# Kernel optimization log

Measured on AMD Instinct MI355X. Metric: run time of the kernel, lower is better.

## Reference

```python
import jax, jax.numpy as jnp
import numpy as np

N = 32768   # nodes
D = 16      # fixed in-degree (neighbors per node)
C = 128     # in_channels
H = 128     # hidden_channels (out of each SAGEConv)


def setup_inputs() -> dict:
    key = jax.random.key(0)
    ks = jax.random.split(key, 20)
    x = jax.random.normal(ks[0], (N, C), dtype=jnp.float32)
    # edges sorted by destination, exactly D neighbors per node (PyG
    # LSTMAggregation requires dst-sorted edge_index)
    src = jax.random.randint(ks[1], (N * D,), 0, N, dtype=jnp.int32)
    dst = jnp.repeat(jnp.arange(N, dtype=jnp.int32), D)
    edge_index = jnp.stack([src, dst])  # [2, E]

    s = 1.0 / np.sqrt(C)
    def mat(k, o, i):
        return jax.random.uniform(k, (o, i), jnp.float32, -s, s)
    def vec(k, o):
        return jax.random.uniform(k, (o,), jnp.float32, -s, s)

    inp = {"x": x, "edge_index": edge_index}
    for k0, base in [(2, "conv1"), (10, "conv2")]:
        inp[f"{base}_wih"] = mat(ks[k0 + 0], 4 * C, C)   # LSTM input weights
        inp[f"{base}_whh"] = mat(ks[k0 + 1], 4 * C, C)   # LSTM hidden weights
        inp[f"{base}_bih"] = vec(ks[k0 + 2], 4 * C)
        inp[f"{base}_bhh"] = vec(ks[k0 + 3], 4 * C)
        inp[f"{base}_wl"] = mat(ks[k0 + 4], H, C)        # lin_l (neighbor branch, has bias)
        inp[f"{base}_bl"] = vec(ks[k0 + 5], H)
        inp[f"{base}_wr"] = mat(ks[k0 + 6], H, C)        # lin_r (root branch, no bias)
    return inp


def _lstm_last(seq, wih, whh, bih, bhh):
    # seq: [D, N, C]. PyTorch LSTM, gate order (i, f, g, o).
    # PyG LSTMAggregation returns lstm(x)[0][:, -1] == hidden state at the
    # last (padded) timestep; here every node has exactly D real neighbors.
    n = seq.shape[1]
    h0 = jnp.zeros((n, wih.shape[0] // 4), seq.dtype)
    b = bih + bhh

    def step(carry, x_t):
        h, c = carry
        g = x_t @ wih.T + h @ whh.T + b            # [N, 4H]
        i, f, gg, o = jnp.split(g, 4, axis=-1)
        c = jax.nn.sigmoid(f) * c + jax.nn.sigmoid(i) * jnp.tanh(gg)
        h = jax.nn.sigmoid(o) * jnp.tanh(c)
        return (h, c), None

    (h, _), _ = jax.lax.scan(step, (h0, h0), seq)
    return h


def _sage_conv(x, src, wih, whh, bih, bhh, wl, bl, wr):
    n, c = x.shape
    d = src.shape[0] // n
    # dense neighbor batch [N, D, C]: edges are dst-sorted with fixed degree,
    # so the gather reshapes directly (== PyG to_dense_batch)
    msgs = x[src].reshape(n, d, c)
    aggr = _lstm_last(jnp.swapaxes(msgs, 0, 1), wih, whh, bih, bhh)  # [N, C]
    return aggr @ wl.T + bl + x @ wr.T


def reference(x, edge_index,
              conv1_wih, conv1_whh, conv1_bih, conv1_bhh, conv1_wl, conv1_bl, conv1_wr,
              conv2_wih, conv2_whh, conv2_bih, conv2_bhh, conv2_wl, conv2_bl, conv2_wr):
    src = edge_index[0]
    h = _sage_conv(x, src, conv1_wih, conv1_whh, conv1_bih, conv1_bhh,
                   conv1_wl, conv1_bl, conv1_wr)
    h = jax.nn.relu(h)
    out = _sage_conv(h, src, conv2_wih, conv2_whh, conv2_bih, conv2_bhh,
                     conv2_wl, conv2_bl, conv2_wr)
    return out
```

## Files before the change

kernel.cpp:

```cpp
#include <hip/hip_runtime.h>
#include <stdint.h>

#define NN 32768
#define DEG 16
#define CH 128
#define G4 512
#define MB 64

typedef short bf16x8 __attribute__((ext_vector_type(8)));
typedef float f32x4 __attribute__((ext_vector_type(4)));
typedef unsigned short u16;
typedef u16 u16x8 __attribute__((ext_vector_type(8)));
typedef uint32_t u32;

#define L2E 1.4426950408889634f

__device__ __forceinline__ u16 f2bf(float f) {
  union { float f; uint32_t u; } v; v.f = f;
  uint32_t u = v.u;
  return (u16)((u + 0x7FFFu + ((u >> 16) & 1u)) >> 16);
}

__device__ __forceinline__ float exp2f_fast(float x) {
#if __has_builtin(__builtin_amdgcn_exp2f)
  return __builtin_amdgcn_exp2f(x);
#else
  float r; asm("v_exp_f32 %0, %1" : "=v"(r) : "v"(x)); return r;
#endif
}
__device__ __forceinline__ float rcpf_fast(float x) {
#if __has_builtin(__builtin_amdgcn_rcpf)
  return __builtin_amdgcn_rcpf(x);
#else
  float r; asm("v_rcp_f32 %0, %1" : "=v"(r) : "v"(x)); return r;
#endif
}
__device__ __forceinline__ u32 cvtpk(float lo, float hi) {
  u32 r; asm("v_cvt_pk_bf16_f32 %0, %1, %2" : "=v"(r) : "v"(lo), "v"(hi));
  return r;
}

__global__ void k_cvt_bf16(const float* __restrict__ in, u16* __restrict__ out, int n8) {
  int i = blockIdx.x * blockDim.x + threadIdx.x;
  if (i >= n8) return;
  const float* pp = in + (size_t)i * 8;
  u16x8 o;
  #pragma unroll
  for (int j = 0; j < 8; ++j) o[j] = f2bf(pp[j]);
  *(u16x8*)(out + (size_t)i * 8) = o;
}

__global__ void k_pack_lstm(const float* __restrict__ wih, const float* __restrict__ whh,
                            const float* __restrict__ bih, const float* __restrict__ bhh,
                            u16* __restrict__ Wc, float* __restrict__ bs) {
  int idx = blockIdx.x * blockDim.x + threadIdx.x;
  int g = idx >> 8, k = idx & 255;
  int gate = g >> 7;
  float sc = (gate == 2) ? (2.0f * L2E) : L2E;
  float v = (k < CH) ? wih[g * CH + k] : whh[g * CH + (k - CH)];
  Wc[g * 256 + k] = f2bf(v * sc);
  if (k == 0) {
    float b = (bih[g] + bhh[g]) * sc;
    bs[g] = (gate == 2) ? b : -b;
  }
}

__global__ void k_pack_lin(const float* __restrict__ wl, const float* __restrict__ wr,
                           u16* __restrict__ W) {
  int idx = blockIdx.x * blockDim.x + threadIdx.x;
  int o = idx >> 8, k = idx & 255;
  float v = (k < CH) ? wl[o * CH + k] : wr[o * CH + (k - CH)];
  W[o * 256 + k] = f2bf(v);
}

__global__ __launch_bounds__(512, 2)
void k_lstm(const u16* __restrict__ xin, const int* __restrict__ src,
            const u16* __restrict__ Wc, const float* __restrict__ bs,
            u16* __restrict__ aggr) {
  __shared__ u16 xh[MB * 256];
  __shared__ int srcs[MB * DEG];
  const int tid = threadIdx.x;
  const int lane = tid & 63;
  const int wave = tid >> 6;
  const int l15 = lane & 15;
  const int lg  = lane >> 4;
  const int nodeBase = blockIdx.x * MB;

  srcs[tid]       = src[nodeBase * DEG + tid];
  srcs[tid + 512] = src[nodeBase * DEG + tid + 512];

  bf16x8 Wf[4][8];
  {
    const u16* wp = Wc + (wave * 16 + l15) * 256 + lg * 8;
    #pragma unroll
    for (int gt = 0; gt < 4; ++gt)
      #pragma unroll
      for (int kt = 0; kt < 8; ++kt)
        Wf[gt][kt] = *(const bf16x8*)(wp + gt * (CH * 256) + kt * 32);
  }
  const float bi = bs[0 * CH + wave * 16 + l15];
  const float bf = bs[1 * CH + wave * 16 + l15];
  const float bg = bs[2 * CH + wave * 16 + l15];
  const float bo = bs[3 * CH + wave * 16 + l15];

  const int s_swz = (l15 & 7) << 4;
  int abase[4];
  #pragma unroll
  for (int mt = 0; mt < 4; ++mt)
    abase[mt] = (mt * 16 + l15) * 512 + ((lg * 16) ^ s_swz);
  int haddr[4];
  #pragma unroll
  for (int q = 0; q < 4; ++q)
    haddr[q] = (lg * 4 + q) * 512 +
               ((256 + wave * 32 + l15 * 2) ^ ((((lg & 1) * 4) + q) << 4));
  const int r  = tid >> 4;
  const int ck = (tid & 15) << 4;
  const int stg  = r * 512 + (ck ^ ((r & 7) << 4));
  const int stgH = r * 512 + ((256 + ck) ^ ((r & 7) << 4));
  const int sidx = r * DEG;

  __syncthreads();
  {
    int s0 = srcs[sidx];
    int s1 = srcs[sidx + 32 * DEG];
    bf16x8 v0 = *(const bf16x8*)(xin + (size_t)s0 * CH + (ck >> 1));
    bf16x8 v1 = *(const bf16x8*)(xin + (size_t)s1 * CH + (ck >> 1));
    *(bf16x8*)((char*)xh + stg)          = v0;
    *(bf16x8*)((char*)xh + stg + 16384)  = v1;
    bf16x8 z = {};
    *(bf16x8*)((char*)xh + stgH)         = z;
    *(bf16x8*)((char*)xh + stgH + 16384) = z;
  }

  float cst[4][4] = {{0.f}};
  u32 hp[4][2];
  const f32x4 zero4 = {0.f, 0.f, 0.f, 0.f};

  #pragma unroll 1
  for (int t = 0; t < DEG; ++t) {
    __syncthreads();
    bf16x8 xp0 = {}, xp1 = {};
    if (t + 1 < DEG) {
      int s0 = srcs[sidx + t + 1];
      int s1 = srcs[sidx + 32 * DEG + t + 1];
      xp0 = *(const bf16x8*)(xin + (size_t)s0 * CH + (ck >> 1));
      xp1 = *(const bf16x8*)(xin + (size_t)s1 * CH + (ck >> 1));
    }
    f32x4 acc[2][4];
    #pragma unroll
    for (int mt = 0; mt < 4; ++mt) {
      const int pp = mt & 1;
      #pragma unroll
      for (int kt = 0; kt < 8; ++kt) {
        bf16x8 A = *(const bf16x8*)((char*)xh + (abase[mt] ^ (kt * 64)));
        if (kt == 0) {
          #pragma unroll
          for (int gt = 0; gt < 4; ++gt)
            acc[pp][gt] = __builtin_amdgcn_mfma_f32_16x16x32_bf16(A, Wf[gt][0], zero4, 0, 0, 0);
        } else {
          #pragma unroll
          for (int gt = 0; gt < 4; ++gt)
            acc[pp][gt] = __builtin_amdgcn_mfma_f32_16x16x32_bf16(A, Wf[gt][kt], acc[pp][gt], 0, 0, 0);
        }
      }
      float hq[4];
      #pragma unroll
      for (int q = 0; q < 4; ++q) {
        float si = rcpf_fast(1.0f + exp2f_fast(bi - acc[pp][0][q]));
        float sf = rcpf_fast(1.0f + exp2f_fast(bf - acc[pp][1][q]));
        float so = rcpf_fast(1.0f + exp2f_fast(bo - acc[pp][3][q]));
        float gg = fmaf(-2.0f, rcpf_fast(1.0f + exp2f_fast(acc[pp][2][q] + bg)), 1.0f);
        float c  = fmaf(sf, cst[mt][q], si * gg);
        cst[mt][q] = c;
        float tc = fmaf(-2.0f, rcpf_fast(1.0f + exp2f_fast(c * 2.8853900817779268f)), 1.0f);
        hq[q] = so * tc;
      }
      hp[mt][0] = cvtpk(hq[0], hq[1]);
      hp[mt][1] = cvtpk(hq[2], hq[3]);
    }
    __syncthreads();
    if (t + 1 < DEG) {
      #pragma unroll
      for (int mt = 0; mt < 4; ++mt) {
        *(u16*)((char*)xh + haddr[0] + mt * 8192) = (u16)(hp[mt][0]);
        *(u16*)((char*)xh + haddr[1] + mt * 8192) = (u16)(hp[mt][0] >> 16);
        *(u16*)((char*)xh + haddr[2] + mt * 8192) = (u16)(hp[mt][1]);
        *(u16*)((char*)xh + haddr[3] + mt * 8192) = (u16)(hp[mt][1] >> 16);
      }
      *(bf16x8*)((char*)xh + stg)         = xp0;
      *(bf16x8*)((char*)xh + stg + 16384) = xp1;
    }
  }

  #pragma unroll
  for (int mt = 0; mt < 4; ++mt) {
    size_t rowb = (size_t)(nodeBase + mt * 16 + lg * 4);
    u16* op = aggr + rowb * CH + wave * 16 + l15;
    op[0 * CH] = (u16)(hp[mt][0]);
    op[1 * CH] = (u16)(hp[mt][0] >> 16);
    op[2 * CH] = (u16)(hp[mt][1]);
    op[3 * CH] = (u16)(hp[mt][1] >> 16);
  }
}

__global__ __launch_bounds__(256, 4)
void k_linear(const u16* __restrict__ aggr, const u16* __restrict__ xroot,
              const u16* __restrict__ W, const float* __restrict__ bl,
              u16* __restrict__ out_bf, float* __restrict__ out_f, int relu) {
  const int lane = threadIdx.x & 63;
  const int wave = threadIdx.x >> 6;
  const int l15 = lane & 15, lg = lane >> 4;
  const int rowBase = blockIdx.x * 64 + wave * 16;

  f32x4 acc[8];
  #pragma unroll
  for (int nt = 0; nt < 8; ++nt) {
    float b = bl[nt * 16 + l15];
    acc[nt] = { b, b, b, b };
  }
  #pragma unroll
  for (int kt = 0; kt < 8; ++kt) {
    const u16* ap = (kt < 4) ? (aggr  + (size_t)(rowBase + l15) * CH + kt * 32 + lg * 8)
                             : (xroot + (size_t)(rowBase + l15) * CH + (kt - 4) * 32 + lg * 8);
    bf16x8 A = *(const bf16x8*)ap;
    #pragma unroll
    for (int nt = 0; nt < 8; ++nt) {
      bf16x8 B = *(const bf16x8*)(W + (nt * 16 + l15) * 256 + kt * 32 + lg * 8);
      acc[nt] = __builtin_amdgcn_mfma_f32_16x16x32_bf16(A, B, acc[nt], 0, 0, 0);
    }
  }
  #pragma unroll
  for (int nt = 0; nt < 8; ++nt) {
    #pragma unroll
    for (int q = 0; q < 4; ++q) {
      float v = acc[nt][q];
      if (relu) v = fmaxf(v, 0.0f);
      int row = rowBase + lg * 4 + q;
      int col = nt * 16 + l15;
      if (out_bf) out_bf[(size_t)row * CH + col] = f2bf(v);
      else        out_f[(size_t)row * CH + col]  = v;
    }
  }
}

extern "C" void kernel_launch(void* const* d_in, const int* in_sizes, int n_in,
                              void* d_out, int out_size, void* d_ws, size_t ws_size,
                              hipStream_t stream) {
  (void)in_sizes; (void)n_in; (void)out_size; (void)ws_size;
  const float* x    = (const float*)d_in[0];
  const int*   ei   = (const int*)d_in[1];
  const float* w1ih = (const float*)d_in[2];
  const float* w1hh = (const float*)d_in[3];
  const float* b1ih = (const float*)d_in[4];
  const float* b1hh = (const float*)d_in[5];
  const float* w1l  = (const float*)d_in[6];
  const float* b1l  = (const float*)d_in[7];
  const float* w1r  = (const float*)d_in[8];
  const float* w2ih = (const float*)d_in[9];
  const float* w2hh = (const float*)d_in[10];
  const float* b2ih = (const float*)d_in[11];
  const float* b2hh = (const float*)d_in[12];
  const float* w2l  = (const float*)d_in[13];
  const float* b2l  = (const float*)d_in[14];
  const float* w2r  = (const float*)d_in[15];

  char* p = (char*)d_ws;
  u16* x_bf  = (u16*)p;  p += (size_t)NN * CH * 2;
  u16* h1_bf = (u16*)p;  p += (size_t)NN * CH * 2;
  u16* ag_bf = (u16*)p;  p += (size_t)NN * CH * 2;
  u16* Wc1   = (u16*)p;  p += G4 * 256 * 2;
  u16* Wc2   = (u16*)p;  p += G4 * 256 * 2;
  u16* Wl1   = (u16*)p;  p += CH * 256 * 2;
  u16* Wl2   = (u16*)p;  p += CH * 256 * 2;
  float* bs1 = (float*)p; p += G4 * 4;
  float* bs2 = (float*)p; p += G4 * 4;

  k_cvt_bf16<<<(NN * CH / 8 + 255) / 256, 256, 0, stream>>>(x, x_bf, NN * CH / 8);
  k_pack_lstm<<<G4, 256, 0, stream>>>(w1ih, w1hh, b1ih, b1hh, Wc1, bs1);
  k_pack_lstm<<<G4, 256, 0, stream>>>(w2ih, w2hh, b2ih, b2hh, Wc2, bs2);
  k_pack_lin<<<CH, 256, 0, stream>>>(w1l, w1r, Wl1);
  k_pack_lin<<<CH, 256, 0, stream>>>(w2l, w2r, Wl2);

  k_lstm<<<NN / MB, 512, 0, stream>>>(x_bf, ei, Wc1, bs1, ag_bf);
  k_linear<<<NN / 64, 256, 0, stream>>>(ag_bf, x_bf, Wl1, b1l, h1_bf, nullptr, 1);
  k_lstm<<<NN / MB, 512, 0, stream>>>(h1_bf, ei, Wc2, bs2, ag_bf);
  k_linear<<<NN / 64, 256, 0, stream>>>(ag_bf, h1_bf, Wl2, b2l, nullptr, (float*)d_out, 0);
}
```

Baseline: 319.1 us.

## Double-buffer LSTM LDS tile to drop one barrier per timestep

Doubles the shared-memory x/h staging buffer so each timestep reads one buffer while writing the next step's hidden state and gathered neighbor features into the other. This removes the second __syncthreads per step and lets each gate block's h be stored as soon as it is computed. The gate bias is folded into the first MFMA accumulator, and s_setprio raises priority around the MFMA loops. The cost is double the LDS per block, which may limit occupancy, plus a fully unrolled macro body that adds code size.

```diff
diff --git a/kernel.cpp b/kernel.cpp
--- a/kernel.cpp
+++ b/kernel.cpp
@@ -6,6 +6,7 @@
 #define CH 128
 #define G4 512
 #define MB 64
+#define BUF 32768
 
 typedef short bf16x8 __attribute__((ext_vector_type(8)));
 typedef float f32x4 __attribute__((ext_vector_type(4)));
@@ -13,14 +14,14 @@
 typedef u16 u16x8 __attribute__((ext_vector_type(8)));
 typedef uint32_t u32;
 
-#define L2E 1.4426950408889634f
+#define L2E  1.4426950408889634f
+#define L2E2 2.8853900817779268f
 
 __device__ __forceinline__ u16 f2bf(float f) {
   union { float f; uint32_t u; } v; v.f = f;
   uint32_t u = v.u;
   return (u16)((u + 0x7FFFu + ((u >> 16) & 1u)) >> 16);
 }
-
 __device__ __forceinline__ float exp2f_fast(float x) {
 #if __has_builtin(__builtin_amdgcn_exp2f)
   return __builtin_amdgcn_exp2f(x);
@@ -56,13 +57,10 @@
   int idx = blockIdx.x * blockDim.x + threadIdx.x;
   int g = idx >> 8, k = idx & 255;
   int gate = g >> 7;
-  float sc = (gate == 2) ? (2.0f * L2E) : L2E;
+  float sc = (gate == 2) ? L2E2 : L2E;
   float v = (k < CH) ? wih[g * CH + k] : whh[g * CH + (k - CH)];
   Wc[g * 256 + k] = f2bf(v * sc);
-  if (k == 0) {
-    float b = (bih[g] + bhh[g]) * sc;
-    bs[g] = (gate == 2) ? b : -b;
-  }
+  if (k == 0) bs[g] = (bih[g] + bhh[g]) * sc;
 }
 
 __global__ void k_pack_lin(const float* __restrict__ wl, const float* __restrict__ wr,
@@ -73,12 +71,76 @@
   W[o * 256 + k] = f2bf(v);
 }
 
+#define LSTM_BODY(T, RD, WR, ISLAST) do {                                      \
+  __syncthreads();                                                             \
+  bf16x8 xp0 = {}, xp1 = {};                                                   \
+  if (!(ISLAST)) {                                                             \
+    int s0_ = srcs[sidx + (T) + 1];                                            \
+    int s1_ = srcs[sidx + 32 * DEG + (T) + 1];                                 \
+    xp0 = *(const bf16x8*)(xin + (size_t)s0_ * CH + ckh);                      \
+    xp1 = *(const bf16x8*)(xin + (size_t)s1_ * CH + ckh);                      \
+  }                                                                            \
+  _Pragma("unroll")                                                            \
+  for (int mt = 0; mt < 4; ++mt) {                                             \
+    const int pp = mt & 1;                                                     \
+    __builtin_amdgcn_s_setprio(1);                                             \
+    _Pragma("unroll")                                                          \
+    for (int kt = 0; kt < 8; ++kt) {                                           \
+      const bf16x8 A = *(const bf16x8*)(xhb + ((kt & 1) ? aB : aA)             \
+                        + ((RD) + mt * 8192 + (kt >> 1) * 128));               \
+      if (kt == 0) {                                                           \
+        _Pragma("unroll")                                                      \
+        for (int gt = 0; gt < 4; ++gt)                                         \
+          acc[pp][gt] = __builtin_amdgcn_mfma_f32_16x16x32_bf16(               \
+              A, Wf[gt][0], bias[gt], 0, 0, 0);                                \
+      } else {                                                                 \
+        _Pragma("unroll")                                                      \
+        for (int gt = 0; gt < 4; ++gt)                                         \
+          acc[pp][gt] = __builtin_amdgcn_mfma_f32_16x16x32_bf16(               \
+              A, Wf[gt][kt], acc[pp][gt], 0, 0, 0);                            \
+      }                                                                        \
+    }                                                                          \
+    __builtin_amdgcn_s_setprio(0);                                             \
+    float hq[4];                                                               \
+    _Pragma("unroll")                                                          \
+    for (int q = 0; q < 4; ++q) {                                              \
+      float si = rcpf_fast(1.0f + exp2f_fast(-acc[pp][0][q]));                 \
+      float sf = rcpf_fast(1.0f + exp2f_fast(-acc[pp][1][q]));                 \
+      float so = rcpf_fast(1.0f + exp2f_fast(-acc[pp][3][q]));                 \
+      float gg = fmaf(-2.0f, rcpf_fast(1.0f + exp2f_fast(acc[pp][2][q])), 1.0f); \
+      float c  = fmaf(sf, cst[mt][q], si * gg);                                \
+      cst[mt][q] = c;                                                          \
+      float tc = fmaf(-2.0f, rcpf_fast(1.0f + exp2f_fast(c * L2E2)), 1.0f);    \
+      hq[q] = so * tc;                                                         \
+    }                                                                          \
+    u32 hp0 = cvtpk(hq[0], hq[1]);                                             \
+    u32 hp1 = cvtpk(hq[2], hq[3]);                                             \
+    if (!(ISLAST)) {                                                           \
+      *(u16*)(xhb + h0a + ((WR) + mt * 8192)) = (u16)hp0;                      \
+      *(u16*)(xhb + h1a + ((WR) + mt * 8192)) = (u16)(hp0 >> 16);              \
+      *(u16*)(xhb + h2a + ((WR) + mt * 8192)) = (u16)hp1;                      \
+      *(u16*)(xhb + h3a + ((WR) + mt * 8192)) = (u16)(hp1 >> 16);              \
+    } else {                                                                   \
+      u16* op_ = aggrp + mt * 16 * CH;                                         \
+      op_[0 * CH] = (u16)hp0;                                                  \
+      op_[1 * CH] = (u16)(hp0 >> 16);                                          \
+      op_[2 * CH] = (u16)hp1;                                                  \
+      op_[3 * CH] = (u16)(hp1 >> 16);                                          \
+    }                                                                          \
+  }                                                                            \
+  if (!(ISLAST)) {                                                             \
+    *(bf16x8*)(xhb + stg + (WR))         = xp0;                                \
+    *(bf16x8*)(xhb + stg + (WR) + 16384) = xp1;                                \
+  }                                                                            \
+} while (0)
+
 __global__ __launch_bounds__(512, 2)
 void k_lstm(const u16* __restrict__ xin, const int* __restrict__ src,
             const u16* __restrict__ Wc, const float* __restrict__ bs,
             u16* __restrict__ aggr) {
-  __shared__ u16 xh[MB * 256];
+  __shared__ u16 xh[2 * MB * 256];
   __shared__ int srcs[MB * DEG];
+  char* xhb = (char*)xh;
   const int tid = threadIdx.x;
   const int lane = tid & 63;
   const int wave = tid >> 6;
@@ -98,109 +160,51 @@
       for (int kt = 0; kt < 8; ++kt)
         Wf[gt][kt] = *(const bf16x8*)(wp + gt * (CH * 256) + kt * 32);
   }
-  const float bi = bs[0 * CH + wave * 16 + l15];
-  const float bf = bs[1 * CH + wave * 16 + l15];
-  const float bg = bs[2 * CH + wave * 16 + l15];
-  const float bo = bs[3 * CH + wave * 16 + l15];
-
-  const int s_swz = (l15 & 7) << 4;
-  int abase[4];
-  #pragma unroll
-  for (int mt = 0; mt < 4; ++mt)
-    abase[mt] = (mt * 16 + l15) * 512 + ((lg * 16) ^ s_swz);
-  int haddr[4];
-  #pragma unroll
-  for (int q = 0; q < 4; ++q)
-    haddr[q] = (lg * 4 + q) * 512 +
-               ((256 + wave * 32 + l15 * 2) ^ ((((lg & 1) * 4) + q) << 4));
-  const int r  = tid >> 4;
-  const int ck = (tid & 15) << 4;
+  f32x4 bias[4];
+  #pragma unroll
+  for (int gt = 0; gt < 4; ++gt) {
+    float b = bs[gt * CH + wave * 16 + l15];
+    bias[gt] = { b, b, b, b };
+  }
+
+  const int aA = l15 * 512 + ((lg * 16) ^ ((l15 & 7) << 4));
+  const int aB = aA ^ 64;
+  const int hcol = 256 + wave * 32 + l15 * 2;
+  const int h0a = (lg * 4 + 0) * 512 + (hcol ^ ((((lg & 1) * 4) + 0) << 4));
+  const int h1a = (lg * 4 + 1) * 512 + (hcol ^ ((((lg & 1) * 4) + 1) << 4));
+  const int h2a = (lg * 4 + 2) * 512 + (hcol ^ ((((lg & 1) * 4) + 2) << 4));
+  const int h3a = (lg * 4 + 3) * 512 + (hcol ^ ((((lg & 1) * 4) + 3) << 4));
+  const int r   = tid >> 4;
+  const int ck  = (tid & 15) << 4;
+  const int ckh = (tid & 15) * 8;
   const int stg  = r * 512 + (ck ^ ((r & 7) << 4));
   const int stgH = r * 512 + ((256 + ck) ^ ((r & 7) << 4));
   const int sidx = r * DEG;
+  u16* aggrp = aggr + (size_t)(nodeBase + lg * 4) * CH + wave * 16 + l15;
 
   __syncthreads();
   {
     int s0 = srcs[sidx];
     int s1 = srcs[sidx + 32 * DEG];
-    bf16x8 v0 = *(const bf16x8*)(xin + (size_t)s0 * CH + (ck >> 1));
-    bf16x8 v1 = *(const bf16x8*)(xin + (size_t)s1 * CH + (ck >> 1));
-    *(bf16x8*)((char*)xh + stg)          = v0;
-    *(bf16x8*)((char*)xh + stg + 16384)  = v1;
+    bf16x8 v0 = *(const bf16x8*)(xin + (size_t)s0 * CH + ckh);
+    bf16x8 v1 = *(const bf16x8*)(xin + (size_t)s1 * CH + ckh);
+    *(bf16x8*)(xhb + stg)          = v0;
+    *(bf16x8*)(xhb + stg + 16384)  = v1;
     bf16x8 z = {};
-    *(bf16x8*)((char*)xh + stgH)         = z;
-    *(bf16x8*)((char*)xh + stgH + 16384) = z;
+    *(bf16x8*)(xhb + stgH)         = z;
+    *(bf16x8*)(xhb + stgH + 16384) = z;
   }
 
   float cst[4][4] = {{0.f}};
-  u32 hp[4][2];
-  const f32x4 zero4 = {0.f, 0.f, 0.f, 0.f};
+  f32x4 acc[2][4];
 
   #pragma unroll 1
-  for (int t = 0; t < DEG; ++t) {
-    __syncthreads();
-    bf16x8 xp0 = {}, xp1 = {};
-    if (t + 1 < DEG) {
-      int s0 = srcs[sidx + t + 1];
-      int s1 = srcs[sidx + 32 * DEG + t + 1];
-      xp0 = *(const bf16x8*)(xin + (size_t)s0 * CH + (ck >> 1));
-      xp1 = *(const bf16x8*)(xin + (size_t)s1 * CH + (ck >> 1));
-    }
-    f32x4 acc[2][4];
-    #pragma unroll
-    for (int mt = 0; mt < 4; ++mt) {
-      const int pp = mt & 1;
-      #pragma unroll
-      for (int kt = 0; kt < 8; ++kt) {
-        bf16x8 A = *(const bf16x8*)((char*)xh + (abase[mt] ^ (kt * 64)));
-        if (kt == 0) {
-          #pragma unroll
-          for (int gt = 0; gt < 4; ++gt)
-            acc[pp][gt] = __builtin_amdgcn_mfma_f32_16x16x32_bf16(A, Wf[gt][0], zero4, 0, 0, 0);
-        } else {
-          #pragma unroll
-          for (int gt = 0; gt < 4; ++gt)
-            acc[pp][gt] = __builtin_amdgcn_mfma_f32_16x16x32_bf16(A, Wf[gt][kt], acc[pp][gt], 0, 0, 0);
-        }
-      }
-      float hq[4];
-      #pragma unroll
-      for (int q = 0; q < 4; ++q) {
-        float si = rcpf_fast(1.0f + exp2f_fast(bi - acc[pp][0][q]));
-        float sf = rcpf_fast(1.0f + exp2f_fast(bf - acc[pp][1][q]));
-        float so = rcpf_fast(1.0f + exp2f_fast(bo - acc[pp][3][q]));
-        float gg = fmaf(-2.0f, rcpf_fast(1.0f + exp2f_fast(acc[pp][2][q] + bg)), 1.0f);
-        float c  = fmaf(sf, cst[mt][q], si * gg);
-        cst[mt][q] = c;
-        float tc = fmaf(-2.0f, rcpf_fast(1.0f + exp2f_fast(c * 2.8853900817779268f)), 1.0f);
-        hq[q] = so * tc;
-      }
-      hp[mt][0] = cvtpk(hq[0], hq[1]);
-      hp[mt][1] = cvtpk(hq[2], hq[3]);
-    }
-    __syncthreads();
-    if (t + 1 < DEG) {
-      #pragma unroll
-      for (int mt = 0; mt < 4; ++mt) {
-        *(u16*)((char*)xh + haddr[0] + mt * 8192) = (u16)(hp[mt][0]);
-        *(u16*)((char*)xh + haddr[1] + mt * 8192) = (u16)(hp[mt][0] >> 16);
-        *(u16*)((char*)xh + haddr[2] + mt * 8192) = (u16)(hp[mt][1]);
-        *(u16*)((char*)xh + haddr[3] + mt * 8192) = (u16)(hp[mt][1] >> 16);
-      }
-      *(bf16x8*)((char*)xh + stg)         = xp0;
-      *(bf16x8*)((char*)xh + stg + 16384) = xp1;
-    }
-  }
-
-  #pragma unroll
-  for (int mt = 0; mt < 4; ++mt) {
-    size_t rowb = (size_t)(nodeBase + mt * 16 + lg * 4);
-    u16* op = aggr + rowb * CH + wave * 16 + l15;
-    op[0 * CH] = (u16)(hp[mt][0]);
-    op[1 * CH] = (u16)(hp[mt][0] >> 16);
-    op[2 * CH] = (u16)(hp[mt][1]);
-    op[3 * CH] = (u16)(hp[mt][1] >> 16);
-  }
+  for (int tp = 0; tp < 7; ++tp) {
+    LSTM_BODY(2 * tp,     0,   BUF, false);
+    LSTM_BODY(2 * tp + 1, BUF, 0,   false);
+  }
+  LSTM_BODY(14, 0,   BUF, false);
+  LSTM_BODY(15, BUF, 0,   true);
 }
 
 __global__ __launch_bounds__(256, 4)
```

Result: no change. 319.9 us (+0.2%).

## Precompute input-gate projections per node and gather them in the LSTM recurrence

Applied to the files above, without the earlier changes.

Because every edge gathers a node feature, the input projection x@Wih is computed once per node (N rows) in a new k_gates kernel and stored as interleaved bf16 gate values. The recurrent kernel then gathers 8-byte gate slices per neighbor instead of feature rows, halving its per-step MFMA K dimension to only the hidden part. It also doubles nodes per block, double-buffers the hidden state in LDS to drop one barrier per step, and folds the bias into the MFMA accumulator. The cost is an extra kernel, a 32 MB gate buffer and a second bf16 rounding of the gate pre-activations.

```diff
diff --git a/kernel.cpp b/kernel.cpp
--- a/kernel.cpp
+++ b/kernel.cpp
@@ -5,7 +5,8 @@
 #define DEG 16
 #define CH 128
 #define G4 512
-#define MB 64
+#define MB 128
+#define BUF 32768
 
 typedef short bf16x8 __attribute__((ext_vector_type(8)));
 typedef float f32x4 __attribute__((ext_vector_type(4)));
@@ -13,14 +14,14 @@
 typedef u16 u16x8 __attribute__((ext_vector_type(8)));
 typedef uint32_t u32;
 
-#define L2E 1.4426950408889634f
+#define L2E  1.4426950408889634f
+#define L2E2 2.8853900817779268f
 
 __device__ __forceinline__ u16 f2bf(float f) {
   union { float f; uint32_t u; } v; v.f = f;
   uint32_t u = v.u;
   return (u16)((u + 0x7FFFu + ((u >> 16) & 1u)) >> 16);
 }
-
 __device__ __forceinline__ float exp2f_fast(float x) {
 #if __has_builtin(__builtin_amdgcn_exp2f)
   return __builtin_amdgcn_exp2f(x);
@@ -56,13 +57,10 @@
   int idx = blockIdx.x * blockDim.x + threadIdx.x;
   int g = idx >> 8, k = idx & 255;
   int gate = g >> 7;
-  float sc = (gate == 2) ? (2.0f * L2E) : L2E;
+  float sc = (gate == 2) ? L2E2 : L2E;
   float v = (k < CH) ? wih[g * CH + k] : whh[g * CH + (k - CH)];
   Wc[g * 256 + k] = f2bf(v * sc);
-  if (k == 0) {
-    float b = (bih[g] + bhh[g]) * sc;
-    bs[g] = (gate == 2) ? b : -b;
-  }
+  if (k == 0) bs[g] = (bih[g] + bhh[g]) * sc;
 }
 
 __global__ void k_pack_lin(const float* __restrict__ wl, const float* __restrict__ wr,
@@ -74,11 +72,61 @@
 }
 
 __global__ __launch_bounds__(512, 2)
-void k_lstm(const u16* __restrict__ xin, const int* __restrict__ src,
+void k_gates(const u16* __restrict__ xin, const u16* __restrict__ Wc,
+             u16* __restrict__ gx) {
+  const int lane = threadIdx.x & 63;
+  const int wave = threadIdx.x >> 6;
+  const int l15 = lane & 15, lg = lane >> 4;
+  const int nodeBase = blockIdx.x * 64;
+
+  bf16x8 B[4][4];
+  int cb[4];
+  #pragma unroll
+  for (int ct = 0; ct < 4; ++ct) {
+    int j = (wave * 4 + ct) * 16 + l15;
+    int wr = ((j & 3) << 7) + (j >> 2);
+    cb[ct] = (j >> 2) * 8 + (j & 3) * 2;
+    #pragma unroll
+    for (int kt = 0; kt < 4; ++kt)
+      B[ct][kt] = *(const bf16x8*)(Wc + wr * 256 + kt * 32 + lg * 8);
+  }
+  char* gxc = (char*)gx;
+  const f32x4 zero4 = {0.f, 0.f, 0.f, 0.f};
+  #pragma unroll
+  for (int mt = 0; mt < 4; ++mt) {
+    bf16x8 A[4];
+    #pragma unroll
+    for (int kt = 0; kt < 4; ++kt)
+      A[kt] = *(const bf16x8*)(xin + (size_t)(nodeBase + mt * 16 + l15) * CH + kt * 32 + lg * 8);
+    f32x4 acc[4] = { zero4, zero4, zero4, zero4 };
+    #pragma unroll
+    for (int kt = 0; kt < 4; ++kt)
+      #pragma unroll
+      for (int ct = 0; ct < 4; ++ct)
+        acc[ct] = __builtin_amdgcn_mfma_f32_16x16x32_bf16(A[kt], B[ct][kt], acc[ct], 0, 0, 0);
+    #pragma unroll
+    for (int ct = 0; ct < 4; ++ct)
+      #pragma unroll
+      for (int q = 0; q < 4; ++q)
+        *(u16*)(gxc + (size_t)(nodeBase + mt * 16 + lg * 4 + q) * 1024 + cb[ct]) =
+            f2bf(acc[ct][q]);
+  }
+}
+
+#define GXISSUE(m) do {                                                        \
+    int4 sv_ = *(const int4*)(ldsc + sTr + (m) * 64);                          \
+    gq[m][0] = *(const uint2*)(gxb + (((u32)sv_.x << 10) + gxoff));            \
+    gq[m][1] = *(const uint2*)(gxb + (((u32)sv_.y << 10) + gxoff));            \
+    gq[m][2] = *(const uint2*)(gxb + (((u32)sv_.z << 10) + gxoff));            \
+    gq[m][3] = *(const uint2*)(gxb + (((u32)sv_.w << 10) + gxoff));            \
+  } while (0)
+
+__global__ __launch_bounds__(512, 2)
+void k_lstm(const u16* __restrict__ gx, const int* __restrict__ src,
             const u16* __restrict__ Wc, const float* __restrict__ bs,
             u16* __restrict__ aggr) {
-  __shared__ u16 xh[MB * 256];
-  __shared__ int srcs[MB * DEG];
+  __shared__ char lds[2 * 32768 + 8192];
+  char* ldsc = lds;
   const int tid = threadIdx.x;
   const int lane = tid & 63;
   const int wave = tid >> 6;
@@ -86,120 +134,121 @@
   const int lg  = lane >> 4;
   const int nodeBase = blockIdx.x * MB;
 
-  srcs[tid]       = src[nodeBase * DEG + tid];
-  srcs[tid + 512] = src[nodeBase * DEG + tid + 512];
-
-  bf16x8 Wf[4][8];
   {
-    const u16* wp = Wc + (wave * 16 + l15) * 256 + lg * 8;
+    int row = tid >> 2, tq = (tid & 3) * 4;
+    int4 s4 = *(const int4*)(src + (size_t)(nodeBase + row) * DEG + tq);
+    int b = 65536 + row * 4;
+    *(int*)(ldsc + b + (tq + 0) * 512) = s4.x;
+    *(int*)(ldsc + b + (tq + 1) * 512) = s4.y;
+    *(int*)(ldsc + b + (tq + 2) * 512) = s4.z;
+    *(int*)(ldsc + b + (tq + 3) * 512) = s4.w;
+  }
+  {
+    int4 z = {0, 0, 0, 0};
+    #pragma unroll
+    for (int j = 0; j < 4; ++j) *(int4*)(ldsc + tid * 64 + j * 16) = z;
+  }
+
+  bf16x8 Wf[4][4];
+  {
+    const u16* wp = Wc + (wave * 16 + l15) * 256 + 128 + lg * 8;
     #pragma unroll
     for (int gt = 0; gt < 4; ++gt)
       #pragma unroll
-      for (int kt = 0; kt < 8; ++kt)
+      for (int kt = 0; kt < 4; ++kt)
         Wf[gt][kt] = *(const bf16x8*)(wp + gt * (CH * 256) + kt * 32);
   }
-  const float bi = bs[0 * CH + wave * 16 + l15];
-  const float bf = bs[1 * CH + wave * 16 + l15];
-  const float bg = bs[2 * CH + wave * 16 + l15];
-  const float bo = bs[3 * CH + wave * 16 + l15];
-
-  const int s_swz = (l15 & 7) << 4;
-  int abase[4];
-  #pragma unroll
-  for (int mt = 0; mt < 4; ++mt)
-    abase[mt] = (mt * 16 + l15) * 512 + ((lg * 16) ^ s_swz);
-  int haddr[4];
-  #pragma unroll
-  for (int q = 0; q < 4; ++q)
-    haddr[q] = (lg * 4 + q) * 512 +
-               ((256 + wave * 32 + l15 * 2) ^ ((((lg & 1) * 4) + q) << 4));
-  const int r  = tid >> 4;
-  const int ck = (tid & 15) << 4;
-  const int stg  = r * 512 + (ck ^ ((r & 7) << 4));
-  const int stgH = r * 512 + ((256 + ck) ^ ((r & 7) << 4));
-  const int sidx = r * DEG;
+  f32x4 bias[4];
+  #pragma unroll
+  for (int gt = 0; gt < 4; ++gt) {
+    float b = bs[gt * CH + wave * 16 + l15];
+    bias[gt] = { b, b, b, b };
+  }
+
+  int aAr = l15 * 256 + ((lg * 16) ^ ((l15 & 7) << 4));
+  int aBr = aAr ^ 64;
+  const int hcol = (wave * 16 + l15) * 2;
+  int hw0 = (lg * 4 + 0) * 256 + (hcol ^ ((((lg * 4) + 0) & 7) << 4)) + BUF;
+  int hw1 = (lg * 4 + 1) * 256 + (hcol ^ ((((lg * 4) + 1) & 7) << 4)) + BUF;
+  int hw2 = (lg * 4 + 2) * 256 + (hcol ^ ((((lg * 4) + 2) & 7) << 4)) + BUF;
+  int hw3 = (lg * 4 + 3) * 256 + (hcol ^ ((((lg * 4) + 3) & 7) << 4)) + BUF;
+  int sTr = 65536 + lg * 16;
+  const u32 gxoff = (u32)(wave * 16 + l15) * 8;
+  const char* gxb = (const char*)gx;
+  u16* aggrp = aggr + (size_t)(nodeBase + lg * 4) * CH + wave * 16 + l15;
+
+  float cst[8][4] = {{0.f}};
+  f32x4 acc[2][4];
 
   __syncthreads();
-  {
-    int s0 = srcs[sidx];
-    int s1 = srcs[sidx + 32 * DEG];
-    bf16x8 v0 = *(const bf16x8*)(xin + (size_t)s0 * CH + (ck >> 1));
-    bf16x8 v1 = *(const bf16x8*)(xin + (size_t)s1 * CH + (ck >> 1));
-    *(bf16x8*)((char*)xh + stg)          = v0;
-    *(bf16x8*)((char*)xh + stg + 16384)  = v1;
-    bf16x8 z = {};
-    *(bf16x8*)((char*)xh + stgH)         = z;
-    *(bf16x8*)((char*)xh + stgH + 16384) = z;
-  }
-
-  float cst[4][4] = {{0.f}};
-  u32 hp[4][2];
-  const f32x4 zero4 = {0.f, 0.f, 0.f, 0.f};
 
   #pragma unroll 1
   for (int t = 0; t < DEG; ++t) {
     __syncthreads();
-    bf16x8 xp0 = {}, xp1 = {};
-    if (t + 1 < DEG) {
-      int s0 = srcs[sidx + t + 1];
-      int s1 = srcs[sidx + 32 * DEG + t + 1];
-      xp0 = *(const bf16x8*)(xin + (size_t)s0 * CH + (ck >> 1));
-      xp1 = *(const bf16x8*)(xin + (size_t)s1 * CH + (ck >> 1));
-    }
-    f32x4 acc[2][4];
-    #pragma unroll
-    for (int mt = 0; mt < 4; ++mt) {
+    uint2 gq[8][4];
+    GXISSUE(0); GXISSUE(1); GXISSUE(2);
+    #pragma unroll
+    for (int mt = 0; mt < 8; ++mt) {
       const int pp = mt & 1;
-      #pragma unroll
-      for (int kt = 0; kt < 8; ++kt) {
-        bf16x8 A = *(const bf16x8*)((char*)xh + (abase[mt] ^ (kt * 64)));
-        if (kt == 0) {
-          #pragma unroll
-          for (int gt = 0; gt < 4; ++gt)
-            acc[pp][gt] = __builtin_amdgcn_mfma_f32_16x16x32_bf16(A, Wf[gt][0], zero4, 0, 0, 0);
-        } else {
-          #pragma unroll
-          for (int gt = 0; gt < 4; ++gt)
-            acc[pp][gt] = __builtin_amdgcn_mfma_f32_16x16x32_bf16(A, Wf[gt][kt], acc[pp][gt], 0, 0, 0);
-        }
+      if (mt < 5) GXISSUE(mt + 3);
+      __builtin_amdgcn_s_setprio(1);
+      {
+        const bf16x8 A0 = *(const bf16x8*)(ldsc + aAr + mt * 4096);
+        const bf16x8 A1 = *(const bf16x8*)(ldsc + aBr + mt * 4096);
+        const bf16x8 A2 = *(const bf16x8*)(ldsc + aAr + mt * 4096 + 128);
+        const bf16x8 A3 = *(const bf16x8*)(ldsc + aBr + mt * 4096 + 128);
+        #pragma unroll
+        for (int gt = 0; gt < 4; ++gt)
+          acc[pp][gt] = __builtin_amdgcn_mfma_f32_16x16x32_bf16(A0, Wf[gt][0], bias[gt], 0, 0, 0);
+        #pragma unroll
+        for (int gt = 0; gt < 4; ++gt)
+          acc[pp][gt] = __builtin_amdgcn_mfma_f32_16x16x32_bf16(A1, Wf[gt][1], acc[pp][gt], 0, 0, 0);
+        #pragma unroll
+        for (int gt = 0; gt < 4; ++gt)
+          acc[pp][gt] = __builtin_amdgcn_mfma_f32_16x16x32_bf16(A2, Wf[gt][2], acc[pp][gt], 0, 0, 0);
+        #pragma unroll
+        for (int gt = 0; gt < 4; ++gt)
+          acc[pp][gt] = __builtin_amdgcn_mfma_f32_16x16x32_bf16(A3, Wf[gt][3], acc[pp][gt], 0, 0, 0);
       }
+      __builtin_amdgcn_s_setprio(0);
       float hq[4];
       #pragma unroll
       for (int q = 0; q < 4; ++q) {
-        float si = rcpf_fast(1.0f + exp2f_fast(bi - acc[pp][0][q]));
-        float sf = rcpf_fast(1.0f + exp2f_fast(bf - acc[pp][1][q]));
-        float so = rcpf_fast(1.0f + exp2f_fast(bo - acc[pp][3][q]));
-        float gg = fmaf(-2.0f, rcpf_fast(1.0f + exp2f_fast(acc[pp][2][q] + bg)), 1.0f);
+        float xi = __uint_as_float(gq[mt][q].x << 16);
+        float xf = __uint_as_float(gq[mt][q].x & 0xFFFF0000u);
+        float xg = __uint_as_float(gq[mt][q].y << 16);
+        float xo = __uint_as_float(gq[mt][q].y & 0xFFFF0000u);
+        float p0 = acc[pp][0][q] + xi;
+        float p1 = acc[pp][1][q] + xf;
+        float p2 = acc[pp][2][q] + xg;
+        float p3 = acc[pp][3][q] + xo;
+        float si = rcpf_fast(1.0f + exp2f_fast(-p0));
+        float sf = rcpf_fast(1.0f + exp2f_fast(-p1));
+        float so = rcpf_fast(1.0f + exp2f_fast(-p3));
+        float gg = fmaf(-2.0f, rcpf_fast(1.0f + exp2f_fast(p2)), 1.0f);
         float c  = fmaf(sf, cst[mt][q], si * gg);
         cst[mt][q] = c;
-        float tc = fmaf(-2.0f, rcpf_fast(1.0f + exp2f_fast(c * 2.8853900817779268f)), 1.0f);
+        float tc = fmaf(-2.0f, rcpf_fast(1.0f + exp2f_fast(c * L2E2)), 1.0f);
         hq[q] = so * tc;
       }
-      hp[mt][0] = cvtpk(hq[0], hq[1]);
-      hp[mt][1] = cvtpk(hq[2], hq[3]);
+      u32 hp0 = cvtpk(hq[0], hq[1]);
+      u32 hp1 = cvtpk(hq[2], hq[3]);
+      if (t != DEG - 1) {
+        *(u16*)(ldsc + hw0 + mt * 4096) = (u16)hp0;
+        *(u16*)(ldsc + hw1 + mt * 4096) = (u16)(hp0 >> 16);
+        *(u16*)(ldsc + hw2 + mt * 4096) = (u16)hp1;
+        *(u16*)(ldsc + hw3 + mt * 4096) = (u16)(hp1 >> 16);
+      } else {
+        u16* op_ = aggrp + mt * 16 * CH;
+        op_[0 * CH] = (u16)hp0;
+        op_[1 * CH] = (u16)(hp0 >> 16);
+        op_[2 * CH] = (u16)hp1;
+        op_[3 * CH] = (u16)(hp1 >> 16);
+      }
     }
-    __syncthreads();
-    if (t + 1 < DEG) {
-      #pragma unroll
-      for (int mt = 0; mt < 4; ++mt) {
-        *(u16*)((char*)xh + haddr[0] + mt * 8192) = (u16)(hp[mt][0]);
-        *(u16*)((char*)xh + haddr[1] + mt * 8192) = (u16)(hp[mt][0] >> 16);
-        *(u16*)((char*)xh + haddr[2] + mt * 8192) = (u16)(hp[mt][1]);
-        *(u16*)((char*)xh + haddr[3] + mt * 8192) = (u16)(hp[mt][1] >> 16);
-      }
-      *(bf16x8*)((char*)xh + stg)         = xp0;
-      *(bf16x8*)((char*)xh + stg + 16384) = xp1;
-    }
-  }
-
-  #pragma unroll
-  for (int mt = 0; mt < 4; ++mt) {
-    size_t rowb = (size_t)(nodeBase + mt * 16 + lg * 4);
-    u16* op = aggr + rowb * CH + wave * 16 + l15;
-    op[0 * CH] = (u16)(hp[mt][0]);
-    op[1 * CH] = (u16)(hp[mt][0] >> 16);
-    op[2 * CH] = (u16)(hp[mt][1]);
-    op[3 * CH] = (u16)(hp[mt][1] >> 16);
+    aAr ^= BUF; aBr ^= BUF;
+    hw0 ^= BUF; hw1 ^= BUF; hw2 ^= BUF; hw3 ^= BUF;
+    sTr += 512;
   }
 }
 
@@ -274,6 +323,7 @@
   u16* Wl2   = (u16*)p;  p += CH * 256 * 2;
   float* bs1 = (float*)p; p += G4 * 4;
   float* bs2 = (float*)p; p += G4 * 4;
+  u16* Gx    = (u16*)p;  p += (size_t)NN * G4 * 2;
 
   k_cvt_bf16<<<(NN * CH / 8 + 255) / 256, 256, 0, stream>>>(x, x_bf, NN * CH / 8);
   k_pack_lstm<<<G4, 256, 0, stream>>>(w1ih, w1hh, b1ih, b1hh, Wc1, bs1);
@@ -281,8 +331,10 @@
   k_pack_lin<<<CH, 256, 0, stream>>>(w1l, w1r, Wl1);
   k_pack_lin<<<CH, 256, 0, stream>>>(w2l, w2r, Wl2);
 
-  k_lstm<<<NN / MB, 512, 0, stream>>>(x_bf, ei, Wc1, bs1, ag_bf);
+  k_gates<<<NN / 64, 512, 0, stream>>>(x_bf, Wc1, Gx);
+  k_lstm<<<NN / MB, 512, 0, stream>>>(Gx, ei, Wc1, bs1, ag_bf);
   k_linear<<<NN / 64, 256, 0, stream>>>(ag_bf, x_bf, Wl1, b1l, h1_bf, nullptr, 1);
-  k_lstm<<<NN / MB, 512, 0, stream>>>(h1_bf, ei, Wc2, bs2, ag_bf);
+  k_gates<<<NN / 64, 512, 0, stream>>>(h1_bf, Wc2, Gx);
+  k_lstm<<<NN / MB, 512, 0, stream>>>(Gx, ei, Wc2, bs2, ag_bf);
   k_linear<<<NN / 64, 256, 0, stream>>>(ag_bf, h1_bf, Wl2, b2l, nullptr, (float*)d_out, 0);
 }
```

After: 331.7 us. 1.04x slower.
